# Kernel optimization log

Measured on AMD Instinct MI355X. Metric: run time of the kernel, lower is better.

Reference implementation:

```python
import jax, jax.numpy as jnp
import numpy as np

D_MODEL = 1024
N_HEAD = 16
B, S = 4, 1024


def setup_inputs() -> dict:
    key = jax.random.key(0)
    ks = jax.random.split(key, 10)
    f = lambda k, shp: jax.random.normal(k, shp, dtype=jnp.float32)
    return {
        "x": f(ks[0], (B, S, D_MODEL)),
        "y": f(ks[1], (B, S, D_MODEL)),
        "z": f(ks[2], (B, S, D_MODEL)),
        "mask": f(ks[3], (1, 1, S, S)) * 0.1,
        "wq_w": f(ks[4], (D_MODEL, D_MODEL)) * (D_MODEL ** -0.5),
        "wq_b": f(ks[5], (D_MODEL,)) * 0.02,
        "wk_w": f(ks[6], (D_MODEL, D_MODEL)) * (D_MODEL ** -0.5),
        "wk_b": f(ks[7], (D_MODEL,)) * 0.02,
        "wv_w": f(ks[8], (D_MODEL, D_MODEL)) * (D_MODEL ** -0.5),
        "wv_b": f(ks[9], (D_MODEL,)) * 0.02,
    }


def reference(x, y, z, mask, wq_w, wq_b, wk_w, wk_b, wv_w, wv_b):
    b, xl, d = x.shape
    hd = d // N_HEAD
    # linear projections (torch Linear: x @ W^T + b)
    q = x @ wq_w.T + wq_b
    k = y @ wk_w.T + wk_b
    v = z @ wv_w.T + wv_b
    # [B, H, L, hd]
    q = q.reshape(b, xl, N_HEAD, hd).transpose(0, 2, 1, 3)
    k = k.reshape(b, y.shape[1], N_HEAD, hd).transpose(0, 2, 1, 3)
    v = v.reshape(b, z.shape[1], N_HEAD, hd).transpose(0, 2, 1, 3)
    # NOTE: source scales by sqrt(d_model), not sqrt(head_dim)
    scale = 1.0 / jnp.sqrt(jnp.asarray(d, dtype=x.dtype))
    logits = jnp.einsum("bhqd,bhkd->bhqk", q, k) * scale
    score = jax.nn.softmax(logits, axis=-1)
    # mask added AFTER softmax (faithful to source)
    score = score + mask
    out = jnp.einsum("bhqk,bhkd->bhqd", score, v)
    return out.transpose(0, 2, 1, 3).reshape(b, xl, d)
```

## Files before the change

### kernel.cpp

```cpp
#include <hip/hip_runtime.h>
#include <hip/hip_bf16.h>
#include <cstdint>

typedef __bf16 bf16_t;
typedef __bf16 bf16x8 __attribute__((ext_vector_type(8)));
typedef __bf16 bf16x4 __attribute__((ext_vector_type(4)));
typedef float floatx4 __attribute__((ext_vector_type(4)));

typedef __attribute__((address_space(3))) uint32_t lds_u32_t;
typedef const __attribute__((address_space(1))) uint32_t g_u32_t;

#define MFMA_BF16(a, b, c) __builtin_amdgcn_mfma_f32_16x16x32_bf16((a), (b), (c), 0, 0, 0)

static constexpr int S = 1024;
static constexpr int HD = 64;

struct ConvArgs {
  const float* src[7];
  bf16_t* dst[7];
  int n[7];
};

__global__ __launch_bounds__(256) void convert_kernel(ConvArgs a) {
  const int j = blockIdx.y;
  const float4* __restrict__ s = (const float4*)a.src[j];
  bf16x4* __restrict__ d = (bf16x4*)a.dst[j];
  const int n4 = a.n[j] >> 2;
  for (int i = blockIdx.x * blockDim.x + threadIdx.x; i < n4; i += gridDim.x * blockDim.x) {
    float4 v = s[i];
    bf16x4 o;
    o[0] = (bf16_t)v.x; o[1] = (bf16_t)v.y; o[2] = (bf16_t)v.z; o[3] = (bf16_t)v.w;
    d[i] = o;
  }
}

struct GemmCfg {
  const bf16_t* A;
  const bf16_t* Bm;
  void* out;
  const float* bias;
  int nbshift;
  int mode;
};

__global__ __launch_bounds__(256) void gemm_nt_kernel(GemmCfg c0, GemmCfg c1, GemmCfg c2, int K) {
  GemmCfg cfg = (blockIdx.y == 0) ? c0 : (blockIdx.y == 1 ? c1 : c2);
  __shared__ bf16_t As[128 * 32];
  __shared__ bf16_t Bs[128 * 32];
  const int tid = threadIdx.x;
  const int wave = tid >> 6;
  const int lane = tid & 63;
  const int g = lane >> 4;
  const int cl = lane & 15;
  const int mq = (wave & 1) * 64;
  const int nq = (wave >> 1) * 64;
  const int nb = blockIdx.x & ((1 << cfg.nbshift) - 1);
  const int mb = blockIdx.x >> cfg.nbshift;
  const int m0 = mb * 128, n0 = nb * 128;

  const bf16_t* Ag = cfg.A + (size_t)(m0 + (tid >> 2)) * K + (tid & 3) * 8;
  const bf16_t* Bg = cfg.Bm + (size_t)(n0 + (tid >> 2)) * K + (tid & 3) * 8;

  floatx4 acc[4][4];
#pragma unroll
  for (int i = 0; i < 4; ++i)
#pragma unroll
    for (int j = 0; j < 4; ++j) acc[i][j] = floatx4{0.f, 0.f, 0.f, 0.f};

  const int kiters = K >> 5;
  for (int kt = 0; kt < kiters; ++kt) {
    __syncthreads();
    __builtin_amdgcn_global_load_lds((g_u32_t*)(const void*)Ag,
                                     (lds_u32_t*)(void*)&As[tid * 8], 16, 0, 0);
    __builtin_amdgcn_global_load_lds((g_u32_t*)(const void*)(Ag + (size_t)64 * K),
                                     (lds_u32_t*)(void*)&As[2048 + tid * 8], 16, 0, 0);
    __builtin_amdgcn_global_load_lds((g_u32_t*)(const void*)Bg,
                                     (lds_u32_t*)(void*)&Bs[tid * 8], 16, 0, 0);
    __builtin_amdgcn_global_load_lds((g_u32_t*)(const void*)(Bg + (size_t)64 * K),
                                     (lds_u32_t*)(void*)&Bs[2048 + tid * 8], 16, 0, 0);
    Ag += 32;
    Bg += 32;
    __syncthreads();

    bf16x8 af[4], bfr[4];
#pragma unroll
    for (int i = 0; i < 4; ++i) af[i] = *(const bf16x8*)&As[(mq + i * 16 + cl) * 32 + g * 8];
#pragma unroll
    for (int j = 0; j < 4; ++j) bfr[j] = *(const bf16x8*)&Bs[(nq + j * 16 + cl) * 32 + g * 8];
#pragma unroll
    for (int i = 0; i < 4; ++i)
#pragma unroll
      for (int j = 0; j < 4; ++j) acc[i][j] = MFMA_BF16(af[i], bfr[j], acc[i][j]);
  }

#pragma unroll
  for (int i = 0; i < 4; ++i) {
#pragma unroll
    for (int j = 0; j < 4; ++j) {
#pragma unroll
      for (int r = 0; r < 4; ++r) {
        const int m = m0 + mq + i * 16 + g * 4 + r;
        const int n = n0 + nq + j * 16 + cl;
        float v = acc[i][j][r];
        if (cfg.mode == 0) {
          v += cfg.bias[n];
          ((bf16_t*)cfg.out)[(size_t)((m >> 10) * 16 + (n >> 6)) * 65536 + (m & 1023) * 64 + (n & 63)] =
              (bf16_t)v;
        } else {
          v += cfg.bias[m];
          ((bf16_t*)cfg.out)[(size_t)((n >> 10) * 16 + (m >> 6)) * 65536 + (m & 63) * 1024 + (n & 1023)] =
              (bf16_t)v;
        }
      }
    }
  }
}

__global__ __launch_bounds__(256, 2) void attn_kernel(const bf16_t* __restrict__ Q,
                                                      const bf16_t* __restrict__ Kb,
                                                      const bf16_t* __restrict__ Vt,
                                                      const bf16_t* __restrict__ Mk,
                                                      float* __restrict__ out) {
  __shared__ bf16_t Ks[128 * 64];
  __shared__ bf16_t Vs[64 * 128];
  __shared__ bf16_t Pbuf[4][32 * 136];
  const int tid = threadIdx.x;
  const int wave = tid >> 6, lane = tid & 63;
  const int g = lane >> 4, cl = lane & 15;
  const int bh = blockIdx.x & 63, qt = blockIdx.x >> 6;
  const int q0w = qt * 128 + wave * 32;
  const bf16_t* Qp = Q + (size_t)bh * (S * HD);
  const bf16_t* Kp = Kb + (size_t)bh * (S * HD);
  const bf16_t* Vp = Vt + (size_t)bh * (S * HD);
  bf16_t* Pw = &Pbuf[wave][0];

  const int krow = tid >> 3, kch = (tid & 7) ^ (krow & 7);
  const int vrow = tid >> 4, vch = (tid & 15) ^ (vrow & 7);
  const int sw = cl & 7;

  bf16x8 qf[2][2];
#pragma unroll
  for (int nj = 0; nj < 2; ++nj)
#pragma unroll
    for (int kc = 0; kc < 2; ++kc)
      qf[nj][kc] = *(const bf16x8*)&Qp[(size_t)(q0w + nj * 16 + cl) * HD + kc * 32 + g * 8];

  floatx4 o[2][4], o2[2][4];
#pragma unroll
  for (int mi = 0; mi < 2; ++mi)
#pragma unroll
    for (int nj = 0; nj < 4; ++nj) {
      o[mi][nj] = floatx4{0.f, 0.f, 0.f, 0.f};
      o2[mi][nj] = floatx4{0.f, 0.f, 0.f, 0.f};
    }
  float dsq[2] = {0.f, 0.f};

  for (int kt = 0; kt < 8; ++kt) {
    const int k0 = kt * 128;
    __syncthreads();
#pragma unroll
    for (int i = 0; i < 4; ++i)
      __builtin_amdgcn_global_load_lds(
          (g_u32_t*)(const void*)&Kp[(size_t)(k0 + i * 32 + krow) * HD + kch * 8],
          (lds_u32_t*)(void*)&Ks[(i * 256 + tid) * 8], 16, 0, 0);
#pragma unroll
    for (int i = 0; i < 4; ++i)
      __builtin_amdgcn_global_load_lds(
          (g_u32_t*)(const void*)&Vp[(size_t)(i * 16 + vrow) * S + k0 + vch * 8],
          (lds_u32_t*)(void*)&Vs[(i * 256 + tid) * 8], 16, 0, 0);
    __syncthreads();

#pragma unroll
    for (int mi = 0; mi < 8; ++mi) {
      bf16x8 kf0 = *(const bf16x8*)&Ks[(mi * 16 + cl) * 64 + ((0 + g) ^ sw) * 8];
      bf16x8 kf1 = *(const bf16x8*)&Ks[(mi * 16 + cl) * 64 + ((4 + g) ^ sw) * 8];
      floatx4 s0 = floatx4{0.f, 0.f, 0.f, 0.f}, s1 = floatx4{0.f, 0.f, 0.f, 0.f};
      s0 = MFMA_BF16(kf0, qf[0][0], s0);
      s0 = MFMA_BF16(kf1, qf[0][1], s0);
      s1 = MFMA_BF16(kf0, qf[1][0], s1);
      s1 = MFMA_BF16(kf1, qf[1][1], s1);
      bf16x4 p0, p1;
#pragma unroll
      for (int r = 0; r < 4; ++r) {
        float e0 = __expf(s0[r] * 0.03125f);
        float e1 = __expf(s1[r] * 0.03125f);
        dsq[0] += e0;
        dsq[1] += e1;
        p0[r] = (bf16_t)e0;
        p1[r] = (bf16_t)e1;
      }
      *(bf16x4*)&Pw[(cl)*136 + mi * 16 + g * 4] = p0;
      *(bf16x4*)&Pw[(16 + cl) * 136 + mi * 16 + g * 4] = p1;
    }

#pragma unroll
    for (int kc = 0; kc < 4; ++kc) {
      bf16x8 pa0 = *(const bf16x8*)&Pw[cl * 136 + kc * 32 + g * 8];
      bf16x8 pa1 = *(const bf16x8*)&Pw[(16 + cl) * 136 + kc * 32 + g * 8];
      bf16x8 ma0 = *(const bf16x8*)&Mk[(size_t)(q0w + cl) * S + k0 + kc * 32 + g * 8];
      bf16x8 ma1 = *(const bf16x8*)&Mk[(size_t)(q0w + 16 + cl) * S + k0 + kc * 32 + g * 8];
#pragma unroll
      for (int nj = 0; nj < 4; ++nj) {
        bf16x8 vf = *(const bf16x8*)&Vs[(nj * 16 + cl) * 128 + ((kc * 4 + g) ^ sw) * 8];
        o[0][nj] = MFMA_BF16(pa0, vf, o[0][nj]);
        o[1][nj] = MFMA_BF16(pa1, vf, o[1][nj]);
        o2[0][nj] = MFMA_BF16(ma0, vf, o2[0][nj]);
        o2[1][nj] = MFMA_BF16(ma1, vf, o2[1][nj]);
      }
    }
  }

#pragma unroll
  for (int nj = 0; nj < 2; ++nj) {
    dsq[nj] += __shfl_xor(dsq[nj], 16, 64);
    dsq[nj] += __shfl_xor(dsq[nj], 32, 64);
  }

  const int b = bh >> 4, h = bh & 15;
#pragma unroll
  for (int mi = 0; mi < 2; ++mi) {
#pragma unroll
    for (int r = 0; r < 4; ++r) {
      float dv = __shfl(dsq[mi], g * 4 + r, 64);
      float dinv = 1.0f / dv;
      const int srow = q0w + mi * 16 + g * 4 + r;
#pragma unroll
      for (int nj = 0; nj < 4; ++nj) {
        const int hd = nj * 16 + cl;
        out[((size_t)b * S + srow) * 1024 + h * HD + hd] = o[mi][nj][r] * dinv + o2[mi][nj][r];
      }
    }
  }
}

extern "C" void kernel_launch(void* const* d_in, const int* in_sizes, int n_in,
                              void* d_out, int out_size, void* d_ws, size_t ws_size,
                              hipStream_t stream) {
  const float* x = (const float*)d_in[0];
  const float* y = (const float*)d_in[1];
  const float* z = (const float*)d_in[2];
  const float* mask = (const float*)d_in[3];
  const float* wq_w = (const float*)d_in[4];
  const float* wq_b = (const float*)d_in[5];
  const float* wk_w = (const float*)d_in[6];
  const float* wk_b = (const float*)d_in[7];
  const float* wv_w = (const float*)d_in[8];
  const float* wv_b = (const float*)d_in[9];

  uint8_t* ws = (uint8_t*)d_ws;
  const size_t MB = 1u << 20;
  bf16_t* Xb = (bf16_t*)(ws + 0 * MB);
  bf16_t* Yb = (bf16_t*)(ws + 8 * MB);
  bf16_t* Zb = (bf16_t*)(ws + 16 * MB);
  bf16_t* Wqb = (bf16_t*)(ws + 24 * MB);
  bf16_t* Wkb = (bf16_t*)(ws + 26 * MB);
  bf16_t* Wvb = (bf16_t*)(ws + 28 * MB);
  bf16_t* Mb = (bf16_t*)(ws + 30 * MB);
  bf16_t* Qb = (bf16_t*)(ws + 32 * MB);
  bf16_t* Kb = (bf16_t*)(ws + 40 * MB);
  bf16_t* Vtb = (bf16_t*)(ws + 48 * MB);

  ConvArgs ca;
  ca.src[0] = x;    ca.dst[0] = Xb;  ca.n[0] = 4 * 1024 * 1024;
  ca.src[1] = y;    ca.dst[1] = Yb;  ca.n[1] = 4 * 1024 * 1024;
  ca.src[2] = z;    ca.dst[2] = Zb;  ca.n[2] = 4 * 1024 * 1024;
  ca.src[3] = wq_w; ca.dst[3] = Wqb; ca.n[3] = 1024 * 1024;
  ca.src[4] = wk_w; ca.dst[4] = Wkb; ca.n[4] = 1024 * 1024;
  ca.src[5] = wv_w; ca.dst[5] = Wvb; ca.n[5] = 1024 * 1024;
  ca.src[6] = mask; ca.dst[6] = Mb;  ca.n[6] = 1024 * 1024;
  convert_kernel<<<dim3(512, 7), 256, 0, stream>>>(ca);

  GemmCfg cq{Xb, Wqb, (void*)Qb, wq_b, 3, 0};
  GemmCfg ck{Yb, Wkb, (void*)Kb, wk_b, 3, 0};
  GemmCfg cv{Wvb, Zb, (void*)Vtb, wv_b, 5, 1};
  gemm_nt_kernel<<<dim3(256, 3), 256, 0, stream>>>(cq, ck, cv, 1024);

  attn_kernel<<<dim3(512), 256, 0, stream>>>(Qb, Kb, Vtb, Mb, (float*)d_out);
}
```

Baseline: 192.2 us.

## Deepen GEMM K-tile, stage epilogue through LDS, and remap blocks per XCD

The projection GEMM now loads 64-wide K tiles instead of 32, which halves the number of barrier pairs per output tile. The epilogue stages biased bf16 results through a padded LDS buffer so the scattered per-element stores become 16-byte coalesced vector stores, and bias is cached in shared memory. Block indices are remapped so that consecutive blocks on the same XCD share A or B rows, aiming for better L2 reuse, and launch bounds request 2 blocks per CU. LDS use grows to about 34KB per block, which may limit occupancy.

```diff
diff --git a/kernel.cpp b/kernel.cpp
--- a/kernel.cpp
+++ b/kernel.cpp
@@ -39,14 +39,18 @@
   const bf16_t* Bm;
   void* out;
   const float* bias;
-  int nbshift;
   int mode;
 };
 
-__global__ __launch_bounds__(256) void gemm_nt_kernel(GemmCfg c0, GemmCfg c1, GemmCfg c2, int K) {
+union GemmSmem {
+  struct { bf16_t A[128 * 64]; bf16_t B[128 * 64]; } ab;
+  bf16_t C[128 * 136];
+};
+
+__global__ __launch_bounds__(256, 2) void gemm_nt_kernel(GemmCfg c0, GemmCfg c1, GemmCfg c2, int K) {
   GemmCfg cfg = (blockIdx.y == 0) ? c0 : (blockIdx.y == 1 ? c1 : c2);
-  __shared__ bf16_t As[128 * 32];
-  __shared__ bf16_t Bs[128 * 32];
+  __shared__ GemmSmem u;
+  __shared__ float bias_s[128];
   const int tid = threadIdx.x;
   const int wave = tid >> 6;
   const int lane = tid & 63;
@@ -54,12 +58,17 @@
   const int cl = lane & 15;
   const int mq = (wave & 1) * 64;
   const int nq = (wave >> 1) * 64;
-  const int nb = blockIdx.x & ((1 << cfg.nbshift) - 1);
-  const int mb = blockIdx.x >> cfg.nbshift;
+
+  const int xcd = blockIdx.x & 7, idx = blockIdx.x >> 3;
+  int mb, nb;
+  if (cfg.mode == 0) { mb = xcd * 4 + (idx & 3); nb = idx >> 2; }
+  else               { nb = xcd * 4 + (idx & 3); mb = idx >> 2; }
   const int m0 = mb * 128, n0 = nb * 128;
 
-  const bf16_t* Ag = cfg.A + (size_t)(m0 + (tid >> 2)) * K + (tid & 3) * 8;
-  const bf16_t* Bg = cfg.Bm + (size_t)(n0 + (tid >> 2)) * K + (tid & 3) * 8;
+  if (tid < 128) bias_s[tid] = cfg.bias[(cfg.mode == 0 ? n0 : m0) + tid];
+
+  const bf16_t* Ag = cfg.A + (size_t)(m0 + (tid >> 3)) * K + (tid & 7) * 8;
+  const bf16_t* Bg = cfg.Bm + (size_t)(n0 + (tid >> 3)) * K + (tid & 7) * 8;
 
   floatx4 acc[4][4];
 #pragma unroll
@@ -67,52 +76,61 @@
 #pragma unroll
     for (int j = 0; j < 4; ++j) acc[i][j] = floatx4{0.f, 0.f, 0.f, 0.f};
 
-  const int kiters = K >> 5;
+  const int kiters = K >> 6;
   for (int kt = 0; kt < kiters; ++kt) {
     __syncthreads();
-    __builtin_amdgcn_global_load_lds((g_u32_t*)(const void*)Ag,
-                                     (lds_u32_t*)(void*)&As[tid * 8], 16, 0, 0);
-    __builtin_amdgcn_global_load_lds((g_u32_t*)(const void*)(Ag + (size_t)64 * K),
-                                     (lds_u32_t*)(void*)&As[2048 + tid * 8], 16, 0, 0);
-    __builtin_amdgcn_global_load_lds((g_u32_t*)(const void*)Bg,
-                                     (lds_u32_t*)(void*)&Bs[tid * 8], 16, 0, 0);
-    __builtin_amdgcn_global_load_lds((g_u32_t*)(const void*)(Bg + (size_t)64 * K),
-                                     (lds_u32_t*)(void*)&Bs[2048 + tid * 8], 16, 0, 0);
-    Ag += 32;
-    Bg += 32;
-    __syncthreads();
-
-    bf16x8 af[4], bfr[4];
-#pragma unroll
-    for (int i = 0; i < 4; ++i) af[i] = *(const bf16x8*)&As[(mq + i * 16 + cl) * 32 + g * 8];
-#pragma unroll
-    for (int j = 0; j < 4; ++j) bfr[j] = *(const bf16x8*)&Bs[(nq + j * 16 + cl) * 32 + g * 8];
-#pragma unroll
-    for (int i = 0; i < 4; ++i)
-#pragma unroll
-      for (int j = 0; j < 4; ++j) acc[i][j] = MFMA_BF16(af[i], bfr[j], acc[i][j]);
-  }
-
-#pragma unroll
-  for (int i = 0; i < 4; ++i) {
-#pragma unroll
-    for (int j = 0; j < 4; ++j) {
+#pragma unroll
+    for (int i = 0; i < 4; ++i) {
+      __builtin_amdgcn_global_load_lds((g_u32_t*)(const void*)(Ag + (size_t)(i * 32) * K),
+                                       (lds_u32_t*)(void*)&u.ab.A[(i * 256 + tid) * 8], 16, 0, 0);
+      __builtin_amdgcn_global_load_lds((g_u32_t*)(const void*)(Bg + (size_t)(i * 32) * K),
+                                       (lds_u32_t*)(void*)&u.ab.B[(i * 256 + tid) * 8], 16, 0, 0);
+    }
+    Ag += 64;
+    Bg += 64;
+    __syncthreads();
+
+#pragma unroll
+    for (int kc = 0; kc < 2; ++kc) {
+      bf16x8 af[4], bfr[4];
+#pragma unroll
+      for (int i = 0; i < 4; ++i)
+        af[i] = *(const bf16x8*)&u.ab.A[(mq + i * 16 + cl) * 64 + kc * 32 + g * 8];
+#pragma unroll
+      for (int j = 0; j < 4; ++j)
+        bfr[j] = *(const bf16x8*)&u.ab.B[(nq + j * 16 + cl) * 64 + kc * 32 + g * 8];
+#pragma unroll
+      for (int i = 0; i < 4; ++i)
+#pragma unroll
+        for (int j = 0; j < 4; ++j) acc[i][j] = MFMA_BF16(af[i], bfr[j], acc[i][j]);
+    }
+  }
+
+  __syncthreads();
+#pragma unroll
+  for (int i = 0; i < 4; ++i)
+#pragma unroll
+    for (int j = 0; j < 4; ++j)
 #pragma unroll
       for (int r = 0; r < 4; ++r) {
-        const int m = m0 + mq + i * 16 + g * 4 + r;
-        const int n = n0 + nq + j * 16 + cl;
-        float v = acc[i][j][r];
-        if (cfg.mode == 0) {
-          v += cfg.bias[n];
-          ((bf16_t*)cfg.out)[(size_t)((m >> 10) * 16 + (n >> 6)) * 65536 + (m & 1023) * 64 + (n & 63)] =
-              (bf16_t)v;
-        } else {
-          v += cfg.bias[m];
-          ((bf16_t*)cfg.out)[(size_t)((n >> 10) * 16 + (m >> 6)) * 65536 + (m & 63) * 1024 + (n & 1023)] =
-              (bf16_t)v;
-        }
-      }
-    }
+        const int ml = mq + i * 16 + g * 4 + r;
+        const int nl = nq + j * 16 + cl;
+        float v = acc[i][j][r] + bias_s[cfg.mode == 0 ? nl : ml];
+        u.C[ml * 136 + nl] = (bf16_t)v;
+      }
+  __syncthreads();
+#pragma unroll
+  for (int it = 0; it < 8; ++it) {
+    const int ix = it * 256 + tid;
+    const int ml = ix >> 4, nc = ix & 15;
+    bf16x8 val = *(const bf16x8*)&u.C[ml * 136 + nc * 8];
+    const int m = m0 + ml, n = n0 + nc * 8;
+    size_t addr;
+    if (cfg.mode == 0)
+      addr = (size_t)((m >> 10) * 16 + (n >> 6)) * 65536 + (m & 1023) * 64 + (n & 63);
+    else
+      addr = (size_t)((n >> 10) * 16 + (m >> 6)) * 65536 + (m & 63) * 1024 + (n & 1023);
+    *(bf16x8*)&((bf16_t*)cfg.out)[addr] = val;
   }
 }
 
@@ -270,9 +288,9 @@
   ca.src[6] = mask; ca.dst[6] = Mb;  ca.n[6] = 1024 * 1024;
   convert_kernel<<<dim3(512, 7), 256, 0, stream>>>(ca);
 
-  GemmCfg cq{Xb, Wqb, (void*)Qb, wq_b, 3, 0};
-  GemmCfg ck{Yb, Wkb, (void*)Kb, wk_b, 3, 0};
-  GemmCfg cv{Wvb, Zb, (void*)Vtb, wv_b, 5, 1};
+  GemmCfg cq{Xb, Wqb, (void*)Qb, wq_b, 0};
+  GemmCfg ck{Yb, Wkb, (void*)Kb, wk_b, 0};
+  GemmCfg cv{Wvb, Zb, (void*)Vtb, wv_b, 1};
   gemm_nt_kernel<<<dim3(256, 3), 256, 0, stream>>>(cq, ck, cv, 1024);
 
   attn_kernel<<<dim3(512), 256, 0, stream>>>(Qb, Kb, Vtb, Mb, (float*)d_out);
```

New measurement: 182.3 us. 1.05x faster.
